# Kernel optimization log

Hardware: AMD Instinct MI355X
Metric: run time of the kernel (lower is better)

The kernel has to match this reference:

```python
import jax, jax.numpy as jnp
import numpy as np

TOP_K = 2


def setup_inputs() -> dict:
    key = jax.random.key(0)
    ks = jax.random.split(key, 7)
    B, S, D, E = 8, 2048, 1024, 8
    scale = 1.0 / np.sqrt(D)
    return {
        "X": jax.random.normal(ks[0], (B, S, D), dtype=jnp.float32),
        "We": jax.random.normal(ks[1], (E, D, D), dtype=jnp.float32) * scale,
        "be": jax.random.normal(ks[2], (E, D), dtype=jnp.float32) * scale,
        "Wr": jax.random.normal(ks[3], (E, D), dtype=jnp.float32) * scale,
        "br": jax.random.normal(ks[4], (E,), dtype=jnp.float32) * scale,
        "Wo": jax.random.normal(ks[5], (D, D), dtype=jnp.float32) * scale,
        "bo": jax.random.normal(ks[6], (D,), dtype=jnp.float32) * scale,
    }


def reference(X, We, be, Wr, br, Wo, bo):
    # Router: logits [B, S, E] -> softmax -> top-k
    router_logits = jnp.einsum("bsd,ed->bse", X, Wr) + br
    router_weights = jax.nn.softmax(router_logits, axis=-1)
    top_k_weights, top_k_indices = jax.lax.top_k(router_weights, TOP_K)  # [B,S,K]

    # Every expert Linear applied to all tokens (matches original's dense-per-expert math).
    # expert_outputs: [B, S, E, D]
    expert_outputs = jnp.einsum("bsd,ehd->bseh", X, We) + be

    # Gather the top-k experts per token and combine with router weights.
    # gathered: [B, S, K, D]
    gathered = jnp.take_along_axis(expert_outputs, top_k_indices[..., None], axis=2)
    combined = jnp.sum(top_k_weights[..., None] * gathered, axis=2)  # [B, S, D]

    # Output projection
    out = jnp.einsum("bsd,hd->bsh", combined, Wo) + bo
    return out
```

## Files before the change

### kernel.cpp

```cpp
#include <hip/hip_runtime.h>
#include <stdint.h>

#define T_TOK 16384
#define D_DIM 1024
#define E_NUM 8
#define NTILE 264

typedef __attribute__((ext_vector_type(4))) float f32x4;
typedef __attribute__((ext_vector_type(8))) __bf16 bf16x8;
typedef __attribute__((ext_vector_type(4))) unsigned short u16x4;
typedef __attribute__((ext_vector_type(8))) unsigned short u16x8;
typedef const __attribute__((address_space(1))) void* gas_ptr;
typedef __attribute__((address_space(3))) void* las_ptr;

#define WS_Y     0ULL
#define WS_ATOK  67108864ULL
#define WS_AW    (WS_ATOK + 131072ULL)
#define WS_ROF   (WS_AW + 131072ULL)
#define WS_TKI   (WS_ROF + 131072ULL)
#define WS_TKW   (WS_TKI + 131072ULL)
#define WS_CNTS  (WS_TKW + 131072ULL)
#define WS_BASE  (WS_CNTS + 8192ULL)
#define WS_SCHED (WS_BASE + 8192ULL)


__device__ __forceinline__ unsigned short f2b(float f){
  unsigned int u = __float_as_uint(f);
  u = (u + 0x7FFFu + ((u >> 16) & 1u)) >> 16;
  return (unsigned short)u;
}
__device__ __forceinline__ float b2f(unsigned short u){
  return __uint_as_float(((unsigned int)u) << 16);
}

__global__ __launch_bounds__(256) void k_router(const float* __restrict__ X,
    const float* __restrict__ Wr, const float* __restrict__ br,
    unsigned short* __restrict__ Xb, int* __restrict__ tki, float* __restrict__ tkw)
{
  const int wv = threadIdx.x >> 6, lane = threadIdx.x & 63;
  const int t = blockIdx.x * 4 + wv;
  const float* x = X + (size_t)t * D_DIM;
  unsigned short* xb = Xb + (size_t)t * D_DIM;
  float acc[E_NUM] = {};
  #pragma unroll
  for (int c = 0; c < 4; ++c){
    const int d = c * 256 + lane * 4;
    f32x4 xv = *reinterpret_cast<const f32x4*>(x + d);
    u16x4 o;
    o[0]=f2b(xv[0]); o[1]=f2b(xv[1]); o[2]=f2b(xv[2]); o[3]=f2b(xv[3]);
    *reinterpret_cast<u16x4*>(xb + d) = o;
    #pragma unroll
    for (int e = 0; e < E_NUM; ++e){
      f32x4 w4 = *reinterpret_cast<const f32x4*>(Wr + e * D_DIM + d);
      acc[e] += xv[0]*w4[0] + xv[1]*w4[1] + xv[2]*w4[2] + xv[3]*w4[3];
    }
  }
  #pragma unroll
  for (int e = 0; e < E_NUM; ++e){
    float v = acc[e];
    #pragma unroll
    for (int off = 32; off >= 1; off >>= 1) v += __shfl_xor(v, off, 64);
    acc[e] = v + br[e];
  }
  int i1 = 0; float l1 = acc[0];
  #pragma unroll
  for (int e = 1; e < E_NUM; ++e) if (acc[e] > l1){ l1 = acc[e]; i1 = e; }
  int i2 = -1; float l2 = -3.4e38f;
  #pragma unroll
  for (int e = 0; e < E_NUM; ++e) if (e != i1 && acc[e] > l2){ l2 = acc[e]; i2 = e; }
  float m = l1, s = 0.f;
  float p1 = 0.f, p2 = 0.f;
  #pragma unroll
  for (int e = 0; e < E_NUM; ++e){ float pe = __expf(acc[e] - m); s += pe; }
  p1 = __expf(l1 - m) / s; p2 = __expf(l2 - m) / s;
  if (lane == 0){
    tki[2*t] = i1; tki[2*t+1] = i2;
    tkw[2*t] = p1; tkw[2*t+1] = p2;
  }
}

__global__ void k_cvt(const float* __restrict__ in, unsigned short* __restrict__ out, int n4)
{
  int i = blockIdx.x * blockDim.x + threadIdx.x;
  if (i >= n4) return;
  f32x4 v = reinterpret_cast<const f32x4*>(in)[i];
  u16x4 o;
  o[0]=f2b(v[0]); o[1]=f2b(v[1]); o[2]=f2b(v[2]); o[3]=f2b(v[3]);
  reinterpret_cast<u16x4*>(out)[i] = o;
}

__global__ __launch_bounds__(64) void k_hist(const int* __restrict__ tki, int* __restrict__ cnts)
{
  const int b = blockIdx.x, lane = threadIdx.x;
  const int t = b * 64 + lane;
  const int e0 = tki[2*t], e1 = tki[2*t+1];
  #pragma unroll
  for (int ex = 0; ex < E_NUM; ++ex){
    unsigned long long m0 = __ballot(e0 == ex);
    unsigned long long m1 = __ballot(e1 == ex);
    if (lane == 0) cnts[b * E_NUM + ex] = __popcll(m0) + __popcll(m1);
  }
}

__global__ __launch_bounds__(64) void k_scan(const int* __restrict__ cnts,
    int* __restrict__ bases, int4* __restrict__ sched)
{
  const int lane = threadIdx.x;
  const int e = lane & 7, g = lane >> 3;
  int own = 0;
  for (int i = 0; i < 32; ++i) own += cnts[(g * 32 + i) * E_NUM + e];
  int incl = own;
  #pragma unroll
  for (int s = 8; s < 64; s <<= 1){
    int v = __shfl_up(incl, s, 64);
    if (lane >= s) incl += v;
  }
  int tot[E_NUM];
  #pragma unroll
  for (int ee = 0; ee < E_NUM; ++ee) tot[ee] = __shfl(incl, 56 + ee, 64);
  int offs_e = 0;
  #pragma unroll
  for (int ee = 0; ee < E_NUM; ++ee) if (ee < e) offs_e += tot[ee];
  int run = offs_e + (incl - own);
  for (int i = 0; i < 32; ++i){
    const int b = g * 32 + i;
    bases[b * E_NUM + e] = run;
    run += cnts[b * E_NUM + e];
  }
  if (lane == 0){
    int slot = 0, off = 0;
    for (int ee = 0; ee < E_NUM; ++ee){
      const int c = tot[ee];
      for (int tile = 0; tile * 128 < c && slot < NTILE; ++tile)
        sched[slot++] = make_int4(ee, off + tile * 128, min(128, c - tile * 128), 0);
      off += c;
    }
    while (slot < NTILE) sched[slot++] = make_int4(0, 0, 0, 0);
  }
}

__global__ __launch_bounds__(64) void k_scatter(const int* __restrict__ tki,
    const float* __restrict__ tkw, const int* __restrict__ bases,
    int* __restrict__ atok, float* __restrict__ aw, int* __restrict__ rof)
{
  const int b = blockIdx.x, lane = threadIdx.x;
  const int t = b * 64 + lane;
  const unsigned long long lt = (1ull << lane) - 1ull;
  const int e0 = tki[2*t], e1 = tki[2*t+1];
  int r0 = 0, r1 = 0, p0c[E_NUM];
  #pragma unroll
  for (int ex = 0; ex < E_NUM; ++ex){
    unsigned long long m0 = __ballot(e0 == ex);
    p0c[ex] = __popcll(m0);
    if (e0 == ex) r0 = __popcll(m0 & lt);
  }
  #pragma unroll
  for (int ex = 0; ex < E_NUM; ++ex){
    unsigned long long m1 = __ballot(e1 == ex);
    if (e1 == ex) r1 = p0c[ex] + __popcll(m1 & lt);
  }
  const int row0 = bases[b * E_NUM + e0] + r0;
  const int row1 = bases[b * E_NUM + e1] + r1;
  atok[row0] = t; aw[row0] = tkw[2*t];   rof[2*t]   = row0;
  atok[row1] = t; aw[row1] = tkw[2*t+1]; rof[2*t+1] = row1;
}

__global__ __launch_bounds__(256) void k_expert(const unsigned short* __restrict__ Xb,
    const unsigned short* __restrict__ Web, const float* __restrict__ be,
    const int4* __restrict__ sched, const int* __restrict__ atok,
    const float* __restrict__ aw, unsigned short* __restrict__ Y)
{
  __shared__ unsigned short As[128 * 64];
  __shared__ unsigned short Bs[128 * 64];
  __shared__ int   tok_s[128];
  __shared__ float w_s[128];

  const int lin = blockIdx.x;
  const int x = lin & 7, c = (lin >> 3) & 7, a = lin >> 6;
  const int j = x * 33 + a;
  const int4 sc = sched[j];
  const int e = sc.x, row0 = sc.y, nval = sc.z;
  const int n0 = c * 128;

  const int tid = threadIdx.x, wv = tid >> 6, lane = tid & 63;
  const int wm = wv >> 1, wn = wv & 1, lr = lane & 15, lg = lane >> 4;

  if (tid < 128){
    tok_s[tid] = atok[row0 + max(0, min(tid, nval - 1))];
    w_s[tid]   = aw[row0 + min(tid, 127)];
  }
  __syncthreads();

  const char* asrc[4]; const char* bsrc[4]; int ldso[4];
  #pragma unroll
  for (int i = 0; i < 4; ++i){
    const int chunk = i * 4 + wv;
    const int byte0 = chunk * 1024 + lane * 16;
    const int r = byte0 >> 7;
    const int cb = byte0 & 127;
    const int scb = cb ^ ((r & 7) << 4);
    asrc[i] = (const char*)(Xb + (size_t)tok_s[r] * D_DIM) + scb;
    bsrc[i] = (const char*)(Web + ((size_t)e * D_DIM + n0 + r) * D_DIM) + scb;
    ldso[i] = chunk * 512;
  }

  f32x4 acc[4][4] = {};
  #pragma unroll 1
  for (int kt = 0; kt < 16; ++kt){
    __syncthreads();
    #pragma unroll
    for (int i = 0; i < 4; ++i){
      __builtin_amdgcn_global_load_lds((gas_ptr)(asrc[i] + kt * 128), (las_ptr)(As + ldso[i]), 16, 0, 0);
      __builtin_amdgcn_global_load_lds((gas_ptr)(bsrc[i] + kt * 128), (las_ptr)(Bs + ldso[i]), 16, 0, 0);
    }
    __syncthreads();
    #pragma unroll
    for (int kk = 0; kk < 2; ++kk){
      bf16x8 af[4], bfr[4];
      #pragma unroll
      for (int fm = 0; fm < 4; ++fm){
        const int r = wm*64 + fm*16 + lr;
        af[fm] = *reinterpret_cast<const bf16x8*>((char*)As + ((r*128 + kk*64 + lg*16) ^ ((r & 7) << 4)));
      }
      #pragma unroll
      for (int fn = 0; fn < 4; ++fn){
        const int r = wn*64 + fn*16 + lr;
        bfr[fn] = *reinterpret_cast<const bf16x8*>((char*)Bs + ((r*128 + kk*64 + lg*16) ^ ((r & 7) << 4)));
      }
      #pragma unroll
      for (int fm = 0; fm < 4; ++fm)
        #pragma unroll
        for (int fn = 0; fn < 4; ++fn)
          acc[fm][fn] = __builtin_amdgcn_mfma_f32_16x16x32_bf16(af[fm], bfr[fn], acc[fm][fn], 0, 0, 0);
    }
  }

  float bev[4];
  #pragma unroll
  for (int fn = 0; fn < 4; ++fn) bev[fn] = be[e * D_DIM + n0 + wn*64 + fn*16 + lr];
  #pragma unroll
  for (int fm = 0; fm < 4; ++fm){
    #pragma unroll
    for (int jj = 0; jj < 4; ++jj){
      const int r = wm*64 + fm*16 + lg*4 + jj;
      if (r < nval){
        const float w = w_s[r];
        #pragma unroll
        for (int fn = 0; fn < 4; ++fn){
          const int col = n0 + wn*64 + fn*16 + lr;
          Y[(size_t)(row0 + r) * D_DIM + col] = f2b(w * (acc[fm][fn][jj] + bev[fn]));
        }
      }
    }
  }
}

__global__ __launch_bounds__(256) void k_outproj(const unsigned short* __restrict__ Y,
    const float* __restrict__ Wo, const int* __restrict__ rof,
    const float* __restrict__ bo, float* __restrict__ out)
{
  __shared__ unsigned short As[128 * 64];
  __shared__ unsigned short Bs[128 * 64];
  __shared__ int ra_s[128], rb_s[128];

  const int lin = blockIdx.x;
  const int x = lin & 7, c = (lin >> 3) & 7, a = lin >> 6;
  const int tm = x * 16 + a;
  const int n0 = c * 128;

  const int tid = threadIdx.x, wv = tid >> 6, lane = tid & 63;
  const int wm = wv >> 1, wn = wv & 1, lr = lane & 15, lg = lane >> 4;

  if (tid < 128){
    const int t = tm * 128 + tid;
    ra_s[tid] = rof[2*t]; rb_s[tid] = rof[2*t+1];
  }
  __syncthreads();

  const int srow = tid >> 3, scol = (tid & 7) * 8;
  const unsigned short* ya[4]; const unsigned short* yb[4]; const float* wo[4];
  #pragma unroll
  for (int p = 0; p < 4; ++p){
    const int r = p * 32 + srow;
    ya[p] = Y + (size_t)ra_s[r] * D_DIM + scol;
    yb[p] = Y + (size_t)rb_s[r] * D_DIM + scol;
    wo[p] = Wo + (size_t)(n0 + r) * D_DIM + scol;
  }

  f32x4 acc[4][4] = {};
  #pragma unroll 1
  for (int kt = 0; kt < 16; ++kt){
    __syncthreads();
    #pragma unroll
    for (int p = 0; p < 4; ++p){
      const int r = p * 32 + srow;
      const int ba = (r * 128 + scol * 2) ^ ((r & 7) << 4);
      u16x8 va = *reinterpret_cast<const u16x8*>(ya[p] + kt * 64);
      u16x8 vb = *reinterpret_cast<const u16x8*>(yb[p] + kt * 64);
      u16x8 o;
      #pragma unroll
      for (int i = 0; i < 8; ++i) o[i] = f2b(b2f(va[i]) + b2f(vb[i]));
      *reinterpret_cast<u16x8*>((char*)As + ba) = o;
      f32x4 b0 = *reinterpret_cast<const f32x4*>(wo[p] + kt * 64);
      f32x4 b1 = *reinterpret_cast<const f32x4*>(wo[p] + kt * 64 + 4);
      u16x8 ob;
      ob[0]=f2b(b0[0]); ob[1]=f2b(b0[1]); ob[2]=f2b(b0[2]); ob[3]=f2b(b0[3]);
      ob[4]=f2b(b1[0]); ob[5]=f2b(b1[1]); ob[6]=f2b(b1[2]); ob[7]=f2b(b1[3]);
      *reinterpret_cast<u16x8*>((char*)Bs + ba) = ob;
    }
    __syncthreads();
    #pragma unroll
    for (int kk = 0; kk < 2; ++kk){
      bf16x8 af[4], bfr[4];
      #pragma unroll
      for (int fm = 0; fm < 4; ++fm){
        const int r = wm*64 + fm*16 + lr;
        af[fm] = *reinterpret_cast<const bf16x8*>((char*)As + ((r*128 + kk*64 + lg*16) ^ ((r & 7) << 4)));
      }
      #pragma unroll
      for (int fn = 0; fn < 4; ++fn){
        const int r = wn*64 + fn*16 + lr;
        bfr[fn] = *reinterpret_cast<const bf16x8*>((char*)Bs + ((r*128 + kk*64 + lg*16) ^ ((r & 7) << 4)));
      }
      #pragma unroll
      for (int fm = 0; fm < 4; ++fm)
        #pragma unroll
        for (int fn = 0; fn < 4; ++fn)
          acc[fm][fn] = __builtin_amdgcn_mfma_f32_16x16x32_bf16(af[fm], bfr[fn], acc[fm][fn], 0, 0, 0);
    }
  }

  float bov[4];
  #pragma unroll
  for (int fn = 0; fn < 4; ++fn) bov[fn] = bo[n0 + wn*64 + fn*16 + lr];
  #pragma unroll
  for (int fm = 0; fm < 4; ++fm){
    #pragma unroll
    for (int jj = 0; jj < 4; ++jj){
      const int r = wm*64 + fm*16 + lg*4 + jj;
      #pragma unroll
      for (int fn = 0; fn < 4; ++fn){
        const int col = n0 + wn*64 + fn*16 + lr;
        out[(size_t)(tm * 128 + r) * D_DIM + col] = acc[fm][fn][jj] + bov[fn];
      }
    }
  }
}

extern "C" void kernel_launch(void* const* d_in, const int* in_sizes, int n_in,
                              void* d_out, int out_size, void* d_ws, size_t ws_size,
                              hipStream_t stream)
{
  const float* X  = (const float*)d_in[0];
  const float* We = (const float*)d_in[1];
  const float* be = (const float*)d_in[2];
  const float* Wr = (const float*)d_in[3];
  const float* br = (const float*)d_in[4];
  const float* Wo = (const float*)d_in[5];
  const float* bo = (const float*)d_in[6];
  float* out = (float*)d_out;
  char* ws = (char*)d_ws;

  unsigned short* Y   = (unsigned short*)(ws + WS_Y);
  int*   atok  = (int*)(ws + WS_ATOK);
  float* aw    = (float*)(ws + WS_AW);
  int*   rof   = (int*)(ws + WS_ROF);
  int*   tki   = (int*)(ws + WS_TKI);
  float* tkw   = (float*)(ws + WS_TKW);
  int*   cnts  = (int*)(ws + WS_CNTS);
  int*   bases = (int*)(ws + WS_BASE);
  int4*  sched = (int4*)(ws + WS_SCHED);

  unsigned short* Xb  = (unsigned short*)d_out;
  unsigned short* Web = (unsigned short*)((char*)d_out + 33554432);

  k_router<<<T_TOK / 4, 256, 0, stream>>>(X, Wr, br, Xb, tki, tkw);
  k_cvt<<<(E_NUM * D_DIM * D_DIM / 4) / 256, 256, 0, stream>>>(We, Web, E_NUM * D_DIM * D_DIM / 4);
  k_hist<<<256, 64, 0, stream>>>(tki, cnts);
  k_scan<<<1, 64, 0, stream>>>(cnts, bases, sched);
  k_scatter<<<256, 64, 0, stream>>>(tki, tkw, bases, atok, aw, rof);
  k_expert<<<NTILE * 8, 256, 0, stream>>>(Xb, Web, be, sched, atok, aw, Y);
  k_outproj<<<1024, 256, 0, stream>>>(Y, Wo, rof, bo, out);
}
```

Baseline: 415.4 us.

## Write expert outputs in token-slot order and stream out-projection via direct LDS loads

New measurement: 352.5 us. -15.1%, faster.

```diff
diff --git a/kernel.cpp b/kernel.cpp
--- a/kernel.cpp
+++ b/kernel.cpp
@@ -9,28 +9,25 @@
 typedef __attribute__((ext_vector_type(4))) float f32x4;
 typedef __attribute__((ext_vector_type(8))) __bf16 bf16x8;
 typedef __attribute__((ext_vector_type(4))) unsigned short u16x4;
-typedef __attribute__((ext_vector_type(8))) unsigned short u16x8;
 typedef const __attribute__((address_space(1))) void* gas_ptr;
 typedef __attribute__((address_space(3))) void* las_ptr;
 
 #define WS_Y     0ULL
 #define WS_ATOK  67108864ULL
 #define WS_AW    (WS_ATOK + 131072ULL)
-#define WS_ROF   (WS_AW + 131072ULL)
-#define WS_TKI   (WS_ROF + 131072ULL)
+#define WS_SCHED (WS_AW + 131072ULL)
+#define WS_TMP   (WS_SCHED + 8192ULL)
+#define WS_TKI   WS_TMP
 #define WS_TKW   (WS_TKI + 131072ULL)
 #define WS_CNTS  (WS_TKW + 131072ULL)
 #define WS_BASE  (WS_CNTS + 8192ULL)
-#define WS_SCHED (WS_BASE + 8192ULL)
+#define WS_WOB   WS_TMP
 
 
 __device__ __forceinline__ unsigned short f2b(float f){
   unsigned int u = __float_as_uint(f);
   u = (u + 0x7FFFu + ((u >> 16) & 1u)) >> 16;
   return (unsigned short)u;
-}
-__device__ __forceinline__ float b2f(unsigned short u){
-  return __uint_as_float(((unsigned int)u) << 16);
 }
 
 __global__ __launch_bounds__(256) void k_router(const float* __restrict__ X,
@@ -68,14 +65,12 @@
   int i2 = -1; float l2 = -3.4e38f;
   #pragma unroll
   for (int e = 0; e < E_NUM; ++e) if (e != i1 && acc[e] > l2){ l2 = acc[e]; i2 = e; }
-  float m = l1, s = 0.f;
-  float p1 = 0.f, p2 = 0.f;
-  #pragma unroll
-  for (int e = 0; e < E_NUM; ++e){ float pe = __expf(acc[e] - m); s += pe; }
-  p1 = __expf(l1 - m) / s; p2 = __expf(l2 - m) / s;
+  float s = 0.f;
+  #pragma unroll
+  for (int e = 0; e < E_NUM; ++e) s += __expf(acc[e] - l1);
   if (lane == 0){
     tki[2*t] = i1; tki[2*t+1] = i2;
-    tkw[2*t] = p1; tkw[2*t+1] = p2;
+    tkw[2*t] = __expf(l1 - l1) / s; tkw[2*t+1] = __expf(l2 - l1) / s;
   }
 }
 
@@ -141,7 +136,7 @@
 
 __global__ __launch_bounds__(64) void k_scatter(const int* __restrict__ tki,
     const float* __restrict__ tkw, const int* __restrict__ bases,
-    int* __restrict__ atok, float* __restrict__ aw, int* __restrict__ rof)
+    int* __restrict__ atok, float* __restrict__ aw)
 {
   const int b = blockIdx.x, lane = threadIdx.x;
   const int t = b * 64 + lane;
@@ -161,8 +156,8 @@
   }
   const int row0 = bases[b * E_NUM + e0] + r0;
   const int row1 = bases[b * E_NUM + e1] + r1;
-  atok[row0] = t; aw[row0] = tkw[2*t];   rof[2*t]   = row0;
-  atok[row1] = t; aw[row1] = tkw[2*t+1]; rof[2*t+1] = row1;
+  atok[row0] = 2*t;     aw[row0] = tkw[2*t];
+  atok[row1] = 2*t + 1; aw[row1] = tkw[2*t+1];
 }
 
 __global__ __launch_bounds__(256) void k_expert(const unsigned short* __restrict__ Xb,
@@ -199,7 +194,7 @@
     const int r = byte0 >> 7;
     const int cb = byte0 & 127;
     const int scb = cb ^ ((r & 7) << 4);
-    asrc[i] = (const char*)(Xb + (size_t)tok_s[r] * D_DIM) + scb;
+    asrc[i] = (const char*)(Xb + (size_t)(tok_s[r] >> 1) * D_DIM) + scb;
     bsrc[i] = (const char*)(Web + ((size_t)e * D_DIM + n0 + r) * D_DIM) + scb;
     ldso[i] = chunk * 512;
   }
@@ -245,10 +240,11 @@
       const int r = wm*64 + fm*16 + lg*4 + jj;
       if (r < nval){
         const float w = w_s[r];
+        const size_t yrow = (size_t)tok_s[r];
         #pragma unroll
         for (int fn = 0; fn < 4; ++fn){
           const int col = n0 + wn*64 + fn*16 + lr;
-          Y[(size_t)(row0 + r) * D_DIM + col] = f2b(w * (acc[fm][fn][jj] + bev[fn]));
+          Y[yrow * D_DIM + col] = f2b(w * (acc[fm][fn][jj] + bev[fn]));
         }
       }
     }
@@ -256,12 +252,12 @@
 }
 
 __global__ __launch_bounds__(256) void k_outproj(const unsigned short* __restrict__ Y,
-    const float* __restrict__ Wo, const int* __restrict__ rof,
-    const float* __restrict__ bo, float* __restrict__ out)
-{
-  __shared__ unsigned short As[128 * 64];
+    const unsigned short* __restrict__ Wob, const float* __restrict__ bo,
+    float* __restrict__ out)
+{
+  __shared__ unsigned short As0[128 * 64];
+  __shared__ unsigned short As1[128 * 64];
   __shared__ unsigned short Bs[128 * 64];
-  __shared__ int ra_s[128], rb_s[128];
 
   const int lin = blockIdx.x;
   const int x = lin & 7, c = (lin >> 3) & 7, a = lin >> 6;
@@ -271,20 +267,19 @@
   const int tid = threadIdx.x, wv = tid >> 6, lane = tid & 63;
   const int wm = wv >> 1, wn = wv & 1, lr = lane & 15, lg = lane >> 4;
 
-  if (tid < 128){
-    const int t = tm * 128 + tid;
-    ra_s[tid] = rof[2*t]; rb_s[tid] = rof[2*t+1];
-  }
-  __syncthreads();
-
-  const int srow = tid >> 3, scol = (tid & 7) * 8;
-  const unsigned short* ya[4]; const unsigned short* yb[4]; const float* wo[4];
-  #pragma unroll
-  for (int p = 0; p < 4; ++p){
-    const int r = p * 32 + srow;
-    ya[p] = Y + (size_t)ra_s[r] * D_DIM + scol;
-    yb[p] = Y + (size_t)rb_s[r] * D_DIM + scol;
-    wo[p] = Wo + (size_t)(n0 + r) * D_DIM + scol;
+  const char* a0src[4]; const char* a1src[4]; const char* bsrc[4]; int ldso[4];
+  #pragma unroll
+  for (int i = 0; i < 4; ++i){
+    const int chunk = i * 4 + wv;
+    const int byte0 = chunk * 1024 + lane * 16;
+    const int r = byte0 >> 7;
+    const int cb = byte0 & 127;
+    const int scb = cb ^ ((r & 7) << 4);
+    const size_t t = (size_t)(tm * 128 + r);
+    a0src[i] = (const char*)(Y + (2*t)     * D_DIM) + scb;
+    a1src[i] = (const char*)(Y + (2*t + 1) * D_DIM) + scb;
+    bsrc[i]  = (const char*)(Wob + (size_t)(n0 + r) * D_DIM) + scb;
+    ldso[i] = chunk * 512;
   }
 
   f32x4 acc[4][4] = {};
@@ -292,30 +287,21 @@
   for (int kt = 0; kt < 16; ++kt){
     __syncthreads();
     #pragma unroll
-    for (int p = 0; p < 4; ++p){
-      const int r = p * 32 + srow;
-      const int ba = (r * 128 + scol * 2) ^ ((r & 7) << 4);
-      u16x8 va = *reinterpret_cast<const u16x8*>(ya[p] + kt * 64);
-      u16x8 vb = *reinterpret_cast<const u16x8*>(yb[p] + kt * 64);
-      u16x8 o;
-      #pragma unroll
-      for (int i = 0; i < 8; ++i) o[i] = f2b(b2f(va[i]) + b2f(vb[i]));
-      *reinterpret_cast<u16x8*>((char*)As + ba) = o;
-      f32x4 b0 = *reinterpret_cast<const f32x4*>(wo[p] + kt * 64);
-      f32x4 b1 = *reinterpret_cast<const f32x4*>(wo[p] + kt * 64 + 4);
-      u16x8 ob;
-      ob[0]=f2b(b0[0]); ob[1]=f2b(b0[1]); ob[2]=f2b(b0[2]); ob[3]=f2b(b0[3]);
-      ob[4]=f2b(b1[0]); ob[5]=f2b(b1[1]); ob[6]=f2b(b1[2]); ob[7]=f2b(b1[3]);
-      *reinterpret_cast<u16x8*>((char*)Bs + ba) = ob;
+    for (int i = 0; i < 4; ++i){
+      __builtin_amdgcn_global_load_lds((gas_ptr)(a0src[i] + kt * 128), (las_ptr)(As0 + ldso[i]), 16, 0, 0);
+      __builtin_amdgcn_global_load_lds((gas_ptr)(a1src[i] + kt * 128), (las_ptr)(As1 + ldso[i]), 16, 0, 0);
+      __builtin_amdgcn_global_load_lds((gas_ptr)(bsrc[i] + kt * 128), (las_ptr)(Bs  + ldso[i]), 16, 0, 0);
     }
     __syncthreads();
     #pragma unroll
     for (int kk = 0; kk < 2; ++kk){
-      bf16x8 af[4], bfr[4];
+      bf16x8 a0f[4], a1f[4], bfr[4];
       #pragma unroll
       for (int fm = 0; fm < 4; ++fm){
         const int r = wm*64 + fm*16 + lr;
-        af[fm] = *reinterpret_cast<const bf16x8*>((char*)As + ((r*128 + kk*64 + lg*16) ^ ((r & 7) << 4)));
+        const int ba = (r*128 + kk*64 + lg*16) ^ ((r & 7) << 4);
+        a0f[fm] = *reinterpret_cast<const bf16x8*>((char*)As0 + ba);
+        a1f[fm] = *reinterpret_cast<const bf16x8*>((char*)As1 + ba);
       }
       #pragma unroll
       for (int fn = 0; fn < 4; ++fn){
@@ -325,8 +311,10 @@
       #pragma unroll
       for (int fm = 0; fm < 4; ++fm)
         #pragma unroll
-        for (int fn = 0; fn < 4; ++fn)
-          acc[fm][fn] = __builtin_amdgcn_mfma_f32_16x16x32_bf16(af[fm], bfr[fn], acc[fm][fn], 0, 0, 0);
+        for (int fn = 0; fn < 4; ++fn){
+          acc[fm][fn] = __builtin_amdgcn_mfma_f32_16x16x32_bf16(a0f[fm], bfr[fn], acc[fm][fn], 0, 0, 0);
+          acc[fm][fn] = __builtin_amdgcn_mfma_f32_16x16x32_bf16(a1f[fm], bfr[fn], acc[fm][fn], 0, 0, 0);
+        }
     }
   }
 
@@ -364,12 +352,12 @@
   unsigned short* Y   = (unsigned short*)(ws + WS_Y);
   int*   atok  = (int*)(ws + WS_ATOK);
   float* aw    = (float*)(ws + WS_AW);
-  int*   rof   = (int*)(ws + WS_ROF);
+  int4*  sched = (int4*)(ws + WS_SCHED);
   int*   tki   = (int*)(ws + WS_TKI);
   float* tkw   = (float*)(ws + WS_TKW);
   int*   cnts  = (int*)(ws + WS_CNTS);
   int*   bases = (int*)(ws + WS_BASE);
-  int4*  sched = (int4*)(ws + WS_SCHED);
+  unsigned short* Wob = (unsigned short*)(ws + WS_WOB);
 
   unsigned short* Xb  = (unsigned short*)d_out;
   unsigned short* Web = (unsigned short*)((char*)d_out + 33554432);
@@ -378,7 +366,8 @@
   k_cvt<<<(E_NUM * D_DIM * D_DIM / 4) / 256, 256, 0, stream>>>(We, Web, E_NUM * D_DIM * D_DIM / 4);
   k_hist<<<256, 64, 0, stream>>>(tki, cnts);
   k_scan<<<1, 64, 0, stream>>>(cnts, bases, sched);
-  k_scatter<<<256, 64, 0, stream>>>(tki, tkw, bases, atok, aw, rof);
+  k_scatter<<<256, 64, 0, stream>>>(tki, tkw, bases, atok, aw);
+  k_cvt<<<(D_DIM * D_DIM / 4) / 256, 256, 0, stream>>>(Wo, Wob, D_DIM * D_DIM / 4);
   k_expert<<<NTILE * 8, 256, 0, stream>>>(Xb, Web, be, sched, atok, aw, Y);
-  k_outproj<<<1024, 256, 0, stream>>>(Y, Wo, rof, bo, out);
-}
+  k_outproj<<<1024, 256, 0, stream>>>(Y, Wob, bo, out);
+}
```
